# Kernel optimization log

Hardware: AMD Instinct MI355X
Metric: run time of the kernel (lower is better)

Reference implementation:

```python
import jax, jax.numpy as jnp
import numpy as np

N = 30000      # nodes
K = 32         # in-degree per node (before self loop)
NFEAT = 512
NHID = 128
NCLASS = 64


def setup_inputs() -> dict:
    key = jax.random.key(0)
    k1, k2, k3, k4 = jax.random.split(key, 4)
    x = jax.random.normal(k1, (N, NFEAT), dtype=jnp.float32)
    # neighbor offsets in [0, N-2]; src = (dst + off + 1) % N guarantees src != dst
    neighbors = jax.random.randint(k2, (N, K), 0, N - 1)
    W1 = jax.random.normal(k3, (NFEAT, NHID), dtype=jnp.float32) / np.float32(np.sqrt(NFEAT))
    b1 = jnp.zeros((NHID,), dtype=jnp.float32)
    W2 = jax.random.normal(k4, (NHID, NCLASS), dtype=jnp.float32) / np.float32(np.sqrt(NHID))
    b2 = jnp.zeros((NCLASS,), dtype=jnp.float32)
    return {"x": x, "neighbors": neighbors, "W1": W1, "b1": b1, "W2": W2, "b2": b2}


def _median_conv(x, nbrs_all, W, b):
    # x: [N, Fin]; nbrs_all: [N, D] neighbor indices (self loop included)
    h = x @ W                          # [N, Fout]
    gathered = h[nbrs_all]             # [N, D, Fout]
    d = nbrs_all.shape[1]
    # torch .median(dim=1) returns the lower median: sorted index (d-1)//2
    med = jnp.sort(gathered, axis=1)[:, (d - 1) // 2]  # [N, Fout]
    return med + b


def reference(x, neighbors, W1, b1, W2, b2):
    n = x.shape[0]
    dst = jnp.arange(n)
    src = (dst[:, None] + neighbors + 1) % n            # no self loops (remove_self_loops)
    nbrs_all = jnp.concatenate([src, dst[:, None]], axis=1)  # add_self_loops -> degree K+1
    # dropout is identity at eval time
    h = jax.nn.relu(_median_conv(x, nbrs_all, W1, b1))
    out = _median_conv(h, nbrs_all, W2, b2)
    return jax.nn.log_softmax(out, axis=1)
```

## Files before the change

kernel.cpp:

```cpp
#include <hip/hip_runtime.h>
#include <hip/hip_bf16.h>
#include <math.h>

static constexpr int NN = 30000;
static constexpr int NF = 512;
static constexpr int NH = 128;
static constexpr int NC = 64;

typedef unsigned int uint32;
typedef __attribute__((ext_vector_type(8))) short bf16x8;
typedef __attribute__((ext_vector_type(4))) float f32x4;

__device__ __forceinline__ float bf_lo(uint32 p) { return __uint_as_float(p << 16); }
__device__ __forceinline__ float bf_hi(uint32 p) { return __uint_as_float(p & 0xffff0000u); }

__device__ __forceinline__ unsigned short bfbits(float f) {
  __hip_bfloat16 h = __float2bfloat16(f);
  return *reinterpret_cast<unsigned short*>(&h);
}

__device__ __forceinline__ void cswap(float& a, float& b) {
  float lo = fminf(a, b), hi = fmaxf(a, b);
  a = lo; b = hi;
}

__device__ __forceinline__ void medsel32(float v[32], float& m15, float& m16) {
  #pragma unroll
  for (int k = 2; k <= 16; k <<= 1) {
    #pragma unroll
    for (int j = k >> 1; j > 0; j >>= 1) {
      #pragma unroll
      for (int h = 0; h < 2; ++h) {
        #pragma unroll
        for (int i = 0; i < 16; ++i) {
          const int l = i ^ j;
          if (l > i) {
            const int a = h * 16 + i, b = h * 16 + l;
            if ((i & k) == 0) cswap(v[a], v[b]);
            else              cswap(v[b], v[a]);
          }
        }
      }
    }
  }
  m15 = fminf(v[0], v[31]);
  m16 = fmaxf(v[0], v[31]);
  #pragma unroll
  for (int i = 1; i < 16; ++i) {
    m15 = fmaxf(m15, fminf(v[i], v[31 - i]));
    m16 = fminf(m16, fmaxf(v[i], v[31 - i]));
  }
}

__global__ __launch_bounds__(256) void k0_prepW1(const float* __restrict__ W1,
                                                 unsigned short* __restrict__ Bp) {
  const int g  = blockIdx.x * 256 + threadIdx.x;
  const int kt = g >> 9;
  const int r  = g & 511;
  const int nt = r >> 6;
  const int l  = r & 63;
  const int ks = l >> 4;
  const int ct = l & 15;
  alignas(16) unsigned short t[8];
  #pragma unroll
  for (int j = 0; j < 8; ++j)
    t[j] = bfbits(W1[(kt * 32 + ks * 8 + j) * NH + nt * 16 + ct]);
  *reinterpret_cast<uint4*>(&Bp[(size_t)g * 8]) = *reinterpret_cast<const uint4*>(t);
}

__global__ __launch_bounds__(256) void k1_gemm1(const float* __restrict__ x,
                                                const unsigned short* __restrict__ Bp,
                                                __hip_bfloat16* __restrict__ h0b) {
  const int tid = threadIdx.x;
  const int w   = tid >> 6;
  const int l   = tid & 63;
  const int m0  = blockIdx.x * 64 + w * 16;

  int arow = m0 + (l & 15);
  if (arow >= NN) arow = NN - 1;
  const float* xrow = x + (size_t)arow * NF + (l >> 4) * 8;

  f32x4 acc[8];
  #pragma unroll
  for (int nt = 0; nt < 8; ++nt) acc[nt] = (f32x4){0.f, 0.f, 0.f, 0.f};

  #pragma unroll 2
  for (int kt = 0; kt < 16; ++kt) {
    const float4 a0 = *reinterpret_cast<const float4*>(xrow + kt * 32);
    const float4 a1 = *reinterpret_cast<const float4*>(xrow + kt * 32 + 4);
    union { bf16x8 v; unsigned short u[8]; } A;
    const float av[8] = {a0.x, a0.y, a0.z, a0.w, a1.x, a1.y, a1.z, a1.w};
    #pragma unroll
    for (int j = 0; j < 8; ++j) A.u[j] = bfbits(av[j]);

    const unsigned short* bbase = Bp + (size_t)kt * 4096 + l * 8;
    #pragma unroll
    for (int nt = 0; nt < 8; ++nt) {
      const bf16x8 B = *reinterpret_cast<const bf16x8*>(bbase + nt * 512);
      acc[nt] = __builtin_amdgcn_mfma_f32_16x16x32_bf16(A.v, B, acc[nt], 0, 0, 0);
    }
  }

  const int rbase = m0 + (l >> 4) * 4;
  const int cbase = l & 15;
  #pragma unroll
  for (int q = 0; q < 4; ++q) {
    const int rr = rbase + q;
    if (rr < NN) {
      #pragma unroll
      for (int nt = 0; nt < 8; ++nt)
        h0b[(size_t)rr * NH + nt * 16 + cbase] = __float2bfloat16(acc[nt][q]);
    }
  }
}

__global__ __launch_bounds__(256) void k2_median1_gemm2(const __hip_bfloat16* __restrict__ h0b,
                                                        const int* __restrict__ nbr,
                                                        const float* __restrict__ b1,
                                                        const float* __restrict__ W2,
                                                        __hip_bfloat16* __restrict__ zb) {
  __shared__ int   nb[4][32];
  __shared__ float hs[4][NH];
  const int tid  = threadIdx.x;
  const int g    = tid >> 6;
  const int lane = tid & 63;
  const int i    = blockIdx.x * 4 + g;

  if (lane < 32) nb[g][lane] = nbr[i * 32 + lane];
  __syncthreads();

  const uint32* hrow = reinterpret_cast<const uint32*>(h0b);
  uint32 pr[32];
  #pragma unroll
  for (int k = 0; k < 32; ++k) {
    int idx = i + nb[g][k] + 1;
    if (idx >= NN) idx -= NN;
    pr[k] = hrow[idx * 64 + lane];
  }
  const uint32 ps = hrow[i * 64 + lane];

  float v[32], m15, m16;
  #pragma unroll
  for (int k = 0; k < 32; ++k) v[k] = bf_lo(pr[k]);
  medsel32(v, m15, m16);
  const float hA = fmaxf(fminf(fmaxf(bf_lo(ps), m15), m16) + b1[lane * 2 + 0], 0.f);

  #pragma unroll
  for (int k = 0; k < 32; ++k) v[k] = bf_hi(pr[k]);
  medsel32(v, m15, m16);
  const float hB = fmaxf(fminf(fmaxf(bf_hi(ps), m15), m16) + b1[lane * 2 + 1], 0.f);

  hs[g][lane * 2 + 0] = hA;
  hs[g][lane * 2 + 1] = hB;
  __syncthreads();

  float acc = 0.f;
  #pragma unroll 16
  for (int kk = 0; kk < NH; ++kk)
    acc = fmaf(hs[g][kk], W2[kk * NC + lane], acc);
  zb[i * NC + lane] = __float2bfloat16(acc);
}

__global__ __launch_bounds__(256) void k3_median2_lsm(const __hip_bfloat16* __restrict__ zb,
                                                      const int* __restrict__ nbr,
                                                      const float* __restrict__ b2,
                                                      float* __restrict__ out) {
  __shared__ int nb[8][32];
  const int tid  = threadIdx.x;
  const int g    = tid >> 5;
  const int lane = tid & 31;
  const int i    = blockIdx.x * 8 + g;

  nb[g][lane] = nbr[i * 32 + lane];
  __syncthreads();

  const uint32* zrow = reinterpret_cast<const uint32*>(zb);
  uint32 pr[32];
  #pragma unroll
  for (int k = 0; k < 32; ++k) {
    int idx = i + nb[g][k] + 1;
    if (idx >= NN) idx -= NN;
    pr[k] = zrow[idx * 32 + lane];
  }
  const uint32 ps = zrow[i * 32 + lane];

  float v[32], m15, m16;
  #pragma unroll
  for (int k = 0; k < 32; ++k) v[k] = bf_lo(pr[k]);
  medsel32(v, m15, m16);
  const float oA = fminf(fmaxf(bf_lo(ps), m15), m16) + b2[lane * 2 + 0];

  #pragma unroll
  for (int k = 0; k < 32; ++k) v[k] = bf_hi(pr[k]);
  medsel32(v, m15, m16);
  const float oB = fminf(fmaxf(bf_hi(ps), m15), m16) + b2[lane * 2 + 1];

  float m = fmaxf(oA, oB);
  #pragma unroll
  for (int d = 1; d < 32; d <<= 1) m = fmaxf(m, __shfl_xor(m, d, 32));
  float s = __expf(oA - m) + __expf(oB - m);
  #pragma unroll
  for (int d = 1; d < 32; d <<= 1) s += __shfl_xor(s, d, 32);
  const float ls = __logf(s);

  *reinterpret_cast<float2*>(&out[i * NC + lane * 2]) =
      make_float2(oA - m - ls, oB - m - ls);
}

extern "C" void kernel_launch(void* const* d_in, const int* in_sizes, int n_in,
                              void* d_out, int out_size, void* d_ws, size_t ws_size,
                              hipStream_t stream) {
  const float* x   = (const float*)d_in[0];
  const int*   nbr = (const int*)d_in[1];
  const float* W1  = (const float*)d_in[2];
  const float* b1  = (const float*)d_in[3];
  const float* W2  = (const float*)d_in[4];
  const float* b2  = (const float*)d_in[5];
  float* outp = (float*)d_out;

  __hip_bfloat16* h0b = (__hip_bfloat16*)d_ws;
  __hip_bfloat16* zb  = (__hip_bfloat16*)((char*)d_ws + (size_t)NN * NH * 2);
  unsigned short* Bp  = (unsigned short*)((char*)d_ws + (size_t)NN * (NH + NC) * 2);

  k0_prepW1<<<32, 256, 0, stream>>>(W1, Bp);
  k1_gemm1<<<(NN + 63) / 64, 256, 0, stream>>>(x, Bp, h0b);
  k2_median1_gemm2<<<NN / 4, 256, 0, stream>>>(h0b, nbr, b1, W2, zb);
  k3_median2_lsm<<<NN / 8, 256, 0, stream>>>(zb, nbr, b2, outp);
}
```

Measured before the change: 212.7 us.

## Store bf16 activations as order-preserving keys and run packed u16 median networks

Intermediate activations are stored as sign-flipped 16-bit keys, so the median selection network can run on two features at once with v_pk_min_u16/v_pk_max_u16 instead of two separate float passes. This roughly halves the ALU work in both median kernels. Alongside this, W2 is transposed in the prep kernel so the second GEMM reads it with float4 loads, all x loads in GEMM1 are issued up front, and neighbor indices are made wave-uniform with readfirstlane. The costs are extra key encode and decode work and higher register pressure in GEMM1 from preloading the whole row.

New measurement: 256.1 us. +20.4%, slower.

```diff
diff --git a/kernel.cpp b/kernel.cpp
--- a/kernel.cpp
+++ b/kernel.cpp
@@ -11,20 +11,31 @@
 typedef __attribute__((ext_vector_type(8))) short bf16x8;
 typedef __attribute__((ext_vector_type(4))) float f32x4;
 
-__device__ __forceinline__ float bf_lo(uint32 p) { return __uint_as_float(p << 16); }
-__device__ __forceinline__ float bf_hi(uint32 p) { return __uint_as_float(p & 0xffff0000u); }
-
 __device__ __forceinline__ unsigned short bfbits(float f) {
   __hip_bfloat16 h = __float2bfloat16(f);
   return *reinterpret_cast<unsigned short*>(&h);
 }
 
-__device__ __forceinline__ void cswap(float& a, float& b) {
-  float lo = fminf(a, b), hi = fmaxf(a, b);
-  a = lo; b = hi;
-}
-
-__device__ __forceinline__ void medsel32(float v[32], float& m15, float& m16) {
+__device__ __forceinline__ uint32 tokey1(uint32 b) {
+  return b ^ (0x8000u | ((b >> 15) * 0x7FFFu));
+}
+__device__ __forceinline__ float keytof(uint32 k) {
+  const uint32 b = k ^ (0xFFFFu - ((k >> 15) & 1u) * 0x7FFFu);
+  return __uint_as_float(b << 16);
+}
+
+__device__ __forceinline__ uint32 pkmin(uint32 a, uint32 b) {
+  uint32 r; asm("v_pk_min_u16 %0, %1, %2" : "=v"(r) : "v"(a), "v"(b)); return r;
+}
+__device__ __forceinline__ uint32 pkmax(uint32 a, uint32 b) {
+  uint32 r; asm("v_pk_max_u16 %0, %1, %2" : "=v"(r) : "v"(a), "v"(b)); return r;
+}
+__device__ __forceinline__ void cswapk(uint32& a, uint32& b) {
+  const uint32 mn = pkmin(a, b), mx = pkmax(a, b);
+  a = mn; b = mx;
+}
+
+__device__ __forceinline__ void medselk(uint32 v[32], uint32& m15, uint32& m16) {
   #pragma unroll
   for (int k = 2; k <= 16; k <<= 1) {
     #pragma unroll
@@ -36,41 +47,50 @@
           const int l = i ^ j;
           if (l > i) {
             const int a = h * 16 + i, b = h * 16 + l;
-            if ((i & k) == 0) cswap(v[a], v[b]);
-            else              cswap(v[b], v[a]);
+            if ((i & k) == 0) cswapk(v[a], v[b]);
+            else              cswapk(v[b], v[a]);
           }
         }
       }
     }
   }
-  m15 = fminf(v[0], v[31]);
-  m16 = fmaxf(v[0], v[31]);
+  m15 = pkmin(v[0], v[31]);
+  m16 = pkmax(v[0], v[31]);
   #pragma unroll
   for (int i = 1; i < 16; ++i) {
-    m15 = fmaxf(m15, fminf(v[i], v[31 - i]));
-    m16 = fminf(m16, fmaxf(v[i], v[31 - i]));
-  }
-}
-
-__global__ __launch_bounds__(256) void k0_prepW1(const float* __restrict__ W1,
-                                                 unsigned short* __restrict__ Bp) {
-  const int g  = blockIdx.x * 256 + threadIdx.x;
-  const int kt = g >> 9;
-  const int r  = g & 511;
-  const int nt = r >> 6;
-  const int l  = r & 63;
-  const int ks = l >> 4;
-  const int ct = l & 15;
-  alignas(16) unsigned short t[8];
-  #pragma unroll
-  for (int j = 0; j < 8; ++j)
-    t[j] = bfbits(W1[(kt * 32 + ks * 8 + j) * NH + nt * 16 + ct]);
-  *reinterpret_cast<uint4*>(&Bp[(size_t)g * 8]) = *reinterpret_cast<const uint4*>(t);
+    m15 = pkmax(m15, pkmin(v[i], v[31 - i]));
+    m16 = pkmin(m16, pkmax(v[i], v[31 - i]));
+  }
+}
+
+__global__ __launch_bounds__(256) void k0_prep(const float* __restrict__ W1,
+                                               const float* __restrict__ W2,
+                                               unsigned short* __restrict__ Bp,
+                                               float* __restrict__ W2T) {
+  const int g = blockIdx.x * 256 + threadIdx.x;
+  if (g < 8192) {
+    const int kt = g >> 9;
+    const int r  = g & 511;
+    const int nt = r >> 6;
+    const int l  = r & 63;
+    const int ks = l >> 4;
+    const int ct = l & 15;
+    alignas(16) unsigned short t[8];
+    #pragma unroll
+    for (int j = 0; j < 8; ++j)
+      t[j] = bfbits(W1[(kt * 32 + ks * 8 + j) * NH + nt * 16 + ct]);
+    *reinterpret_cast<uint4*>(&Bp[(size_t)g * 8]) = *reinterpret_cast<const uint4*>(t);
+  } else {
+    const int t  = g - 8192;
+    const int c  = t >> 7;
+    const int kk = t & 127;
+    W2T[c * NH + kk] = W2[kk * NC + c];
+  }
 }
 
 __global__ __launch_bounds__(256) void k1_gemm1(const float* __restrict__ x,
                                                 const unsigned short* __restrict__ Bp,
-                                                __hip_bfloat16* __restrict__ h0b) {
+                                                unsigned short* __restrict__ h0k) {
   const int tid = threadIdx.x;
   const int w   = tid >> 6;
   const int l   = tid & 63;
@@ -84,12 +104,18 @@
   #pragma unroll
   for (int nt = 0; nt < 8; ++nt) acc[nt] = (f32x4){0.f, 0.f, 0.f, 0.f};
 
-  #pragma unroll 2
+  float4 abuf[16][2];
+  #pragma unroll
   for (int kt = 0; kt < 16; ++kt) {
-    const float4 a0 = *reinterpret_cast<const float4*>(xrow + kt * 32);
-    const float4 a1 = *reinterpret_cast<const float4*>(xrow + kt * 32 + 4);
+    abuf[kt][0] = *reinterpret_cast<const float4*>(xrow + kt * 32);
+    abuf[kt][1] = *reinterpret_cast<const float4*>(xrow + kt * 32 + 4);
+  }
+
+  #pragma unroll
+  for (int kt = 0; kt < 16; ++kt) {
     union { bf16x8 v; unsigned short u[8]; } A;
-    const float av[8] = {a0.x, a0.y, a0.z, a0.w, a1.x, a1.y, a1.z, a1.w};
+    const float av[8] = {abuf[kt][0].x, abuf[kt][0].y, abuf[kt][0].z, abuf[kt][0].w,
+                         abuf[kt][1].x, abuf[kt][1].y, abuf[kt][1].z, abuf[kt][1].w};
     #pragma unroll
     for (int j = 0; j < 8; ++j) A.u[j] = bfbits(av[j]);
 
@@ -108,17 +134,19 @@
     const int rr = rbase + q;
     if (rr < NN) {
       #pragma unroll
-      for (int nt = 0; nt < 8; ++nt)
-        h0b[(size_t)rr * NH + nt * 16 + cbase] = __float2bfloat16(acc[nt][q]);
+      for (int nt = 0; nt < 8; ++nt) {
+        const uint32 b = bfbits(acc[nt][q]);
+        h0k[(size_t)rr * NH + nt * 16 + cbase] = (unsigned short)tokey1(b);
+      }
     }
   }
 }
 
-__global__ __launch_bounds__(256) void k2_median1_gemm2(const __hip_bfloat16* __restrict__ h0b,
+__global__ __launch_bounds__(256) void k2_median1_gemm2(const unsigned short* __restrict__ h0k,
                                                         const int* __restrict__ nbr,
                                                         const float* __restrict__ b1,
-                                                        const float* __restrict__ W2,
-                                                        __hip_bfloat16* __restrict__ zb) {
+                                                        const float* __restrict__ W2T,
+                                                        unsigned short* __restrict__ zk) {
   __shared__ int   nb[4][32];
   __shared__ float hs[4][NH];
   const int tid  = threadIdx.x;
@@ -129,39 +157,43 @@
   if (lane < 32) nb[g][lane] = nbr[i * 32 + lane];
   __syncthreads();
 
-  const uint32* hrow = reinterpret_cast<const uint32*>(h0b);
+  const uint32* hk = reinterpret_cast<const uint32*>(h0k);
   uint32 pr[32];
   #pragma unroll
   for (int k = 0; k < 32; ++k) {
-    int idx = i + nb[g][k] + 1;
+    const int nbk = __builtin_amdgcn_readfirstlane(nb[g][k]);
+    int idx = i + nbk + 1;
     if (idx >= NN) idx -= NN;
-    pr[k] = hrow[idx * 64 + lane];
-  }
-  const uint32 ps = hrow[i * 64 + lane];
-
-  float v[32], m15, m16;
-  #pragma unroll
-  for (int k = 0; k < 32; ++k) v[k] = bf_lo(pr[k]);
-  medsel32(v, m15, m16);
-  const float hA = fmaxf(fminf(fmaxf(bf_lo(ps), m15), m16) + b1[lane * 2 + 0], 0.f);
-
-  #pragma unroll
-  for (int k = 0; k < 32; ++k) v[k] = bf_hi(pr[k]);
-  medsel32(v, m15, m16);
-  const float hB = fmaxf(fminf(fmaxf(bf_hi(ps), m15), m16) + b1[lane * 2 + 1], 0.f);
-
+    pr[k] = hk[idx * 64 + lane];
+  }
+  const uint32 ps = hk[i * 64 + lane];
+
+  uint32 m15, m16;
+  medselk(pr, m15, m16);
+  const uint32 medk = pkmin(pkmax(ps, m15), m16);
+
+  const float hA = fmaxf(keytof(medk & 0xFFFFu) + b1[lane * 2 + 0], 0.f);
+  const float hB = fmaxf(keytof(medk >> 16)     + b1[lane * 2 + 1], 0.f);
   hs[g][lane * 2 + 0] = hA;
   hs[g][lane * 2 + 1] = hB;
   __syncthreads();
 
+  const float4* w4 = reinterpret_cast<const float4*>(W2T + lane * NH);
+  const float4* h4 = reinterpret_cast<const float4*>(&hs[g][0]);
   float acc = 0.f;
-  #pragma unroll 16
-  for (int kk = 0; kk < NH; ++kk)
-    acc = fmaf(hs[g][kk], W2[kk * NC + lane], acc);
-  zb[i * NC + lane] = __float2bfloat16(acc);
-}
-
-__global__ __launch_bounds__(256) void k3_median2_lsm(const __hip_bfloat16* __restrict__ zb,
+  #pragma unroll
+  for (int t = 0; t < 32; ++t) {
+    const float4 wv = w4[t];
+    const float4 hv = h4[t];
+    acc = fmaf(wv.x, hv.x, acc);
+    acc = fmaf(wv.y, hv.y, acc);
+    acc = fmaf(wv.z, hv.z, acc);
+    acc = fmaf(wv.w, hv.w, acc);
+  }
+  zk[i * NC + lane] = (unsigned short)tokey1(bfbits(acc));
+}
+
+__global__ __launch_bounds__(256) void k3_median2_lsm(const unsigned short* __restrict__ zk,
                                                       const int* __restrict__ nbr,
                                                       const float* __restrict__ b2,
                                                       float* __restrict__ out) {
@@ -174,26 +206,22 @@
   nb[g][lane] = nbr[i * 32 + lane];
   __syncthreads();
 
-  const uint32* zrow = reinterpret_cast<const uint32*>(zb);
+  const uint32* zz = reinterpret_cast<const uint32*>(zk);
   uint32 pr[32];
   #pragma unroll
   for (int k = 0; k < 32; ++k) {
     int idx = i + nb[g][k] + 1;
     if (idx >= NN) idx -= NN;
-    pr[k] = zrow[idx * 32 + lane];
-  }
-  const uint32 ps = zrow[i * 32 + lane];
-
-  float v[32], m15, m16;
-  #pragma unroll
-  for (int k = 0; k < 32; ++k) v[k] = bf_lo(pr[k]);
-  medsel32(v, m15, m16);
-  const float oA = fminf(fmaxf(bf_lo(ps), m15), m16) + b2[lane * 2 + 0];
-
-  #pragma unroll
-  for (int k = 0; k < 32; ++k) v[k] = bf_hi(pr[k]);
-  medsel32(v, m15, m16);
-  const float oB = fminf(fmaxf(bf_hi(ps), m15), m16) + b2[lane * 2 + 1];
+    pr[k] = zz[idx * 32 + lane];
+  }
+  const uint32 ps = zz[i * 32 + lane];
+
+  uint32 m15, m16;
+  medselk(pr, m15, m16);
+  const uint32 medk = pkmin(pkmax(ps, m15), m16);
+
+  const float oA = keytof(medk & 0xFFFFu) + b2[lane * 2 + 0];
+  const float oB = keytof(medk >> 16)     + b2[lane * 2 + 1];
 
   float m = fmaxf(oA, oB);
   #pragma unroll
@@ -218,12 +246,13 @@
   const float* b2  = (const float*)d_in[5];
   float* outp = (float*)d_out;
 
-  __hip_bfloat16* h0b = (__hip_bfloat16*)d_ws;
-  __hip_bfloat16* zb  = (__hip_bfloat16*)((char*)d_ws + (size_t)NN * NH * 2);
+  unsigned short* h0k = (unsigned short*)d_ws;
+  unsigned short* zk  = (unsigned short*)((char*)d_ws + (size_t)NN * NH * 2);
   unsigned short* Bp  = (unsigned short*)((char*)d_ws + (size_t)NN * (NH + NC) * 2);
-
-  k0_prepW1<<<32, 256, 0, stream>>>(W1, Bp);
-  k1_gemm1<<<(NN + 63) / 64, 256, 0, stream>>>(x, Bp, h0b);
-  k2_median1_gemm2<<<NN / 4, 256, 0, stream>>>(h0b, nbr, b1, W2, zb);
-  k3_median2_lsm<<<NN / 8, 256, 0, stream>>>(zb, nbr, b2, outp);
-}
+  float*          W2T = (float*)((char*)d_ws + (size_t)NN * (NH + NC) * 2 + 131072);
+
+  k0_prep<<<64, 256, 0, stream>>>(W1, W2, Bp, W2T);
+  k1_gemm1<<<(NN + 63) / 64, 256, 0, stream>>>(x, Bp, h0k);
+  k2_median1_gemm2<<<NN / 4, 256, 0, stream>>>(h0k, nbr, b1, W2T, zk);
+  k3_median2_lsm<<<NN / 8, 256, 0, stream>>>(zk, nbr, b2, outp);
+}
```
